# Kernel optimization log

Measured on AMD Instinct MI355X. Metric: run time of the kernel, lower is better.

The kernel has to match this reference:

```python
import jax, jax.numpy as jnp
import numpy as np

L, D, V, BS, H, HD, DL = 12, 768, 50257, 1024, 12, 64, 256
B, T = 2, 1024
EPS = 1e-5


def _ln(x, w, b):
    m = jnp.mean(x, axis=-1, keepdims=True)
    v = jnp.mean((x - m) ** 2, axis=-1, keepdims=True)
    return (x - m) * jax.lax.rsqrt(v + EPS) * w + b


def _rope_tables(t_len):
    inv_freq = 1.0 / (10000.0 ** (jnp.arange(0, HD, 2, dtype=jnp.float32) / HD))
    t = jnp.arange(t_len, dtype=jnp.float32)
    freqs = jnp.outer(t, inv_freq)  # [T, HD/2]
    return jnp.cos(freqs), jnp.sin(freqs)


def _apply_rope(x, cos, sin):
    # x: [B, H, T, HD]; cos/sin: [T, HD/2]
    c = jnp.concatenate([cos, cos], axis=-1)[None, None]
    s = jnp.concatenate([sin, sin], axis=-1)[None, None]
    x1, x2 = jnp.split(x, 2, axis=-1)
    rot = jnp.concatenate([-x2, x1], axis=-1)
    return x * c + rot * s


def setup_inputs() -> dict:
    key = jax.random.key(0)
    ks = jax.random.split(key, 16)
    std = 0.02
    n = lambda k, shape: jax.random.normal(k, shape, dtype=jnp.float32) * std
    return {
        'idx': jax.random.randint(ks[0], (B, T), 0, V),
        'wte': n(ks[1], (V, D)),
        'wpe': n(ks[2], (BS, D)),
        'ln1_w': jnp.ones((L, D)), 'ln1_b': jnp.zeros((L, D)),
        'wq_w': n(ks[3], (L, D, H * HD)), 'wq_b': jnp.zeros((L, H * HD)),
        'kva_w': n(ks[4], (L, D, DL)), 'kva_b': jnp.zeros((L, DL)),
        'kvb_w': n(ks[5], (L, DL, 2 * H * HD)), 'kvb_b': jnp.zeros((L, 2 * H * HD)),
        'out_w': n(ks[6], (L, H * HD, D)), 'out_b': jnp.zeros((L, D)),
        'ln2_w': jnp.ones((L, D)), 'ln2_b': jnp.zeros((L, D)),
        'fc_w': n(ks[7], (L, D, 4 * D)), 'fc_b': jnp.zeros((L, 4 * D)),
        'proj_w': n(ks[8], (L, 4 * D, D)), 'proj_b': jnp.zeros((L, D)),
        'lnf_w': jnp.ones((D,)), 'lnf_b': jnp.zeros((D,)),
    }


def _forward(idx, wte, wpe, ln1_w, ln1_b, wq_w, wq_b, kva_w, kva_b, kvb_w, kvb_b,
             out_w, out_b, ln2_w, ln2_b, fc_w, fc_b, proj_w, proj_b, lnf_w, lnf_b):
    b, t = idx.shape
    x = wte[idx] + wpe[:t][None]  # [B,T,D]
    cos, sin = _rope_tables(t)
    scale = 1.0 / np.sqrt(HD)
    causal = jnp.tril(jnp.ones((t, t), dtype=bool))
    for l in range(L):
        h = _ln(x, ln1_w[l], ln1_b[l])
        q = (h @ wq_w[l] + wq_b[l]).reshape(b, t, H, HD).transpose(0, 2, 1, 3)
        kv_latent = h @ kva_w[l] + kva_b[l]  # [B,T,DL] (the cacheable latent)
        kv = (kv_latent @ kvb_w[l] + kvb_b[l]).reshape(b, t, 2, H, HD)
        kv = kv.transpose(2, 0, 3, 1, 4)  # [2,B,H,T,HD]
        k, v = kv[0], kv[1]
        q = _apply_rope(q, cos, sin)
        k = _apply_rope(k, cos, sin)
        scores = jnp.einsum('bhtd,bhsd->bhts', q, k) * scale
        scores = jnp.where(causal[None, None], scores, -jnp.inf)
        probs = jax.nn.softmax(scores, axis=-1)
        attn = jnp.einsum('bhts,bhsd->bhtd', probs, v)
        attn = attn.transpose(0, 2, 1, 3).reshape(b, t, H * HD)
        x = x + attn @ out_w[l] + out_b[l]
        h2 = _ln(x, ln2_w[l], ln2_b[l])
        mlp = jax.nn.gelu(h2 @ fc_w[l] + fc_b[l], approximate=False) @ proj_w[l] + proj_b[l]
        x = x + mlp
    x = _ln(x, lnf_w, lnf_b)
    logits = x @ wte.T  # tied lm_head
    return logits


def reference(idx, wte, wpe, ln1_w, ln1_b, wq_w, wq_b, kva_w, kva_b, kvb_w, kvb_b,
              out_w, out_b, ln2_w, ln2_b, fc_w, fc_b, proj_w, proj_b, lnf_w, lnf_b):
    return _forward(idx, wte, wpe, ln1_w, ln1_b, wq_w, wq_b, kva_w, kva_b, kvb_w,
                    kvb_b, out_w, out_b, ln2_w, ln2_b, fc_w, fc_b, proj_w, proj_b,
                    lnf_w, lnf_b)
```

## Files before the change

kernel.cpp:

```cpp
#include <hip/hip_runtime.h>
#include <cstdint>
#include <cstddef>


typedef unsigned short ushortT;
typedef __bf16 bf16x8 __attribute__((ext_vector_type(8)));
typedef float f32x4 __attribute__((ext_vector_type(4)));

#define NHEAD 12
#define T_SEQ 1024

__device__ __forceinline__ float bf2f(unsigned short u) {
    union { unsigned int i; float f; } v; v.i = ((unsigned int)u) << 16; return v.f;
}
__device__ __forceinline__ unsigned short f2bf(float f) {
    union { float f; unsigned int i; } v; v.f = f;
    unsigned int r = v.i + 0x7fffu + ((v.i >> 16) & 1u);
    return (unsigned short)(r >> 16);
}
__device__ __forceinline__ unsigned int pack2(float a, float b) {
    return (unsigned int)f2bf(a) | ((unsigned int)f2bf(b) << 16);
}
__device__ __forceinline__ void gload_lds16(const void* g, void* l) {
    __builtin_amdgcn_global_load_lds((__attribute__((address_space(1))) void*)g,
                                     (__attribute__((address_space(3))) void*)l, 16, 0, 0);
}
template <int N>
__device__ __forceinline__ void wait_vmcnt() {
    if constexpr (N == 8)      asm volatile("s_waitcnt vmcnt(8)" ::: "memory");
    else if constexpr (N == 6) asm volatile("s_waitcnt vmcnt(6)" ::: "memory");
    else if constexpr (N == 4) asm volatile("s_waitcnt vmcnt(4)" ::: "memory");
    else                       asm volatile("s_waitcnt vmcnt(0)" ::: "memory");
}

__global__ __launch_bounds__(256) void transpose_cvt_kernel(
    const float* __restrict__ in, ushortT* __restrict__ outp,
    int K, int N, int outRowOff, size_t outLS) {
    __shared__ float tile[32][33];
    const int tid = threadIdx.x;
    const int n0 = blockIdx.x * 32, k0 = blockIdx.y * 32;
    const float* src = in + (size_t)blockIdx.z * K * N;
    {
        const int r = tid >> 3, cg = tid & 7;
        float4 v = *(const float4*)(src + (size_t)(k0 + r) * N + n0 + cg * 4);
        tile[r][cg * 4 + 0] = v.x; tile[r][cg * 4 + 1] = v.y;
        tile[r][cg * 4 + 2] = v.z; tile[r][cg * 4 + 3] = v.w;
    }
    __syncthreads();
    {
        const int nr = tid >> 3, kg = tid & 7;
        ushort4 o;
        o.x = f2bf(tile[kg * 4 + 0][nr]);
        o.y = f2bf(tile[kg * 4 + 1][nr]);
        o.z = f2bf(tile[kg * 4 + 2][nr]);
        o.w = f2bf(tile[kg * 4 + 3][nr]);
        ushortT* dst = outp + (size_t)blockIdx.z * outLS;
        *(ushort4*)(dst + (size_t)(outRowOff + n0 + nr) * K + k0 + kg * 4) = o;
    }
}

__global__ void cvt_wte_kernel(const float* __restrict__ in, ushortT* __restrict__ outp) {
    size_t i4 = (size_t)blockIdx.x * 256 + threadIdx.x;
    ushort4 o;
    if (i4 < 9649344) {
        float4 v = ((const float4*)in)[i4];
        o.x = f2bf(v.x); o.y = f2bf(v.y); o.z = f2bf(v.z); o.w = f2bf(v.w);
    } else { o.x = 0; o.y = 0; o.z = 0; o.w = 0; }
    ((ushort4*)outp)[i4] = o;
}

__global__ void embed_kernel(const int* __restrict__ idx, const float* __restrict__ wte,
                             const float* __restrict__ wpe, float* __restrict__ x) {
    int i = blockIdx.x * 256 + threadIdx.x;
    int row = i / 768, d = i - row * 768;
    int t = row & 1023;
    x[i] = wte[(size_t)idx[row] * 768 + d] + wpe[(size_t)t * 768 + d];
}

__global__ void rope_tables_kernel(float* __restrict__ cosT, float* __restrict__ sinT) {
    int i = blockIdx.x * 256 + threadIdx.x;
    int t = i >> 5, f = i & 31;
    float invf = exp2f(-(float)f * (13.287712379549449f / 32.0f));
    float ang = (float)t * invf;
    cosT[i] = cosf(ang);
    sinT[i] = sinf(ang);
}

__global__ __launch_bounds__(256) void ln_kernel(const float* __restrict__ x,
                                                 const float* __restrict__ wg,
                                                 const float* __restrict__ bg,
                                                 ushortT* __restrict__ outp) {
    const int row = blockIdx.x, tid = threadIdx.x;
    const float* xr = x + (size_t)row * 768;
    float v0 = xr[tid], v1 = xr[tid + 256], v2 = xr[tid + 512];
    float s = v0 + v1 + v2;
    float ss = v0 * v0 + v1 * v1 + v2 * v2;
#pragma unroll
    for (int off = 32; off >= 1; off >>= 1) {
        s += __shfl_xor(s, off);
        ss += __shfl_xor(ss, off);
    }
    __shared__ float sb[4], ssb[4];
    if ((tid & 63) == 0) { sb[tid >> 6] = s; ssb[tid >> 6] = ss; }
    __syncthreads();
    float S = sb[0] + sb[1] + sb[2] + sb[3];
    float SS = ssb[0] + ssb[1] + ssb[2] + ssb[3];
    const float mean = S * (1.0f / 768.0f);
    float var = SS * (1.0f / 768.0f) - mean * mean;
    const float rs = rsqrtf(var + 1e-5f);
    ushortT* orow = outp + (size_t)row * 768;
    orow[tid]       = f2bf((v0 - mean) * rs * wg[tid]       + bg[tid]);
    orow[tid + 256] = f2bf((v1 - mean) * rs * wg[tid + 256] + bg[tid + 256]);
    orow[tid + 512] = f2bf((v2 - mean) * rs * wg[tid + 512] + bg[tid + 512]);
}

template <int BM, int NF, int NTHR, bool ROPE>
__global__ __launch_bounds__(NTHR) void gemmT(
    const ushortT* __restrict__ A, int lda,
    const ushortT* __restrict__ Bt, int ldb,
    int K, int CS, int Nstore,
    const float* __restrict__ bias0, const float* __restrict__ bias1,
    ushortT* __restrict__ outB0, int ld0,
    ushortT* __restrict__ outB1, int ld1, int mode1,
    const float* __restrict__ resid, float* __restrict__ outF, int ldF,
    int act, const float* __restrict__ cosT, const float* __restrict__ sinT) {
    constexpr int WC = (NTHR == 512) ? 4 : 2;
    constexpr int WMR = BM / 2;
    constexpr int MF = WMR / 16;
    constexpr int NFh = NF / WC;
    constexpr int WNh = NFh * 16;
    constexpr int ABYTES = BM * 128;
    constexpr int BBYTES = NF * 2048;
    constexpr int BUFB = ABYTES + BBYTES;
    constexpr int A_LOADS = (BM * 8) / NTHR;
    constexpr int B_LOADS = (NF * 128) / NTHR;
    constexpr int S = A_LOADS + B_LOADS;
    __shared__ __align__(16) char lds[2 * BUFB];
    const int tid = threadIdx.x;
    const int w = tid >> 6, lane = tid & 63;
    const int wm = w / WC, wn = w % WC;
    const int gx = gridDim.x;
    const int nwg = gx * gridDim.y;
    const int flat = blockIdx.x + gx * blockIdx.y;
    const int xcd = flat & 7, loc = flat >> 3;
    const int qq = nwg >> 3, rr_ = nwg & 7;
    const int swz = (xcd < rr_ ? xcd * (qq + 1) : rr_ * (qq + 1) + (xcd - rr_) * qq) + loc;
    const int m0 = (swz % gx) * BM, n0 = (swz / gx) * NF * 16;
    const int fr = lane & 15, kg = lane >> 4;
    const size_t ldaB = (size_t)lda * 2, ldbB = (size_t)ldb * 2;
    const char* Ab = (const char*)A;
    const char* Bb = (const char*)Bt;
    f32x4 acc[MF][NFh] = {};

    auto stage = [&](int buf, int t) {
        const size_t ktB = (size_t)t << 7;
        char* As_ = lds + buf * BUFB;
        char* Bs_ = As_ + ABYTES;
#pragma unroll
        for (int jj = 0; jj < A_LOADS; ++jj) {
            const int i = tid + jj * NTHR;
            const int r = i >> 3, c = i & 7, cc = c ^ (r & 7);
            gload_lds16(Ab + (size_t)(m0 + r) * ldaB + ktB + cc * 16, As_ + i * 16);
        }
#pragma unroll
        for (int jj = 0; jj < B_LOADS; ++jj) {
            const int i = tid + jj * NTHR;
            const int r = i >> 3, c = i & 7, cc = c ^ (r & 7);
            gload_lds16(Bb + (size_t)(n0 + r) * ldbB + ktB + cc * 16, Bs_ + i * 16);
        }
    };

    const int nk = K >> 6;
    stage(0, 0);
    if (nk > 1) { stage(1, 1); wait_vmcnt<S>(); }
    else        { wait_vmcnt<0>(); }
    __builtin_amdgcn_s_barrier();

    for (int t = 0; t < nk; ++t) {
        const int cur = t & 1;
        const char* As_ = lds + cur * BUFB;
        const char* Bs_ = As_ + ABYTES;
        bf16x8 af[MF][2], bfr[NFh][2];
#pragma unroll
        for (int mf = 0; mf < MF; ++mf) {
            const int row = wm * WMR + mf * 16 + fr;
#pragma unroll
            for (int ks = 0; ks < 2; ++ks)
                af[mf][ks] = *(const bf16x8*)(As_ + row * 128 + (((ks * 4 + kg) ^ (row & 7)) << 4));
        }
#pragma unroll
        for (int nf = 0; nf < NFh; ++nf) {
            const int row = wn * WNh + nf * 16 + fr;
#pragma unroll
            for (int ks = 0; ks < 2; ++ks)
                bfr[nf][ks] = *(const bf16x8*)(Bs_ + row * 128 + (((ks * 4 + kg) ^ (row & 7)) << 4));
        }
        if (t + 2 < nk) {
            asm volatile("s_waitcnt lgkmcnt(0)" ::: "memory");
            __builtin_amdgcn_s_barrier();
            stage(cur, t + 2);
        }
#pragma unroll
        for (int ks = 0; ks < 2; ++ks)
#pragma unroll
            for (int nf = 0; nf < NFh; ++nf)
#pragma unroll
                for (int mf = 0; mf < MF; ++mf)
                    acc[mf][nf] = __builtin_amdgcn_mfma_f32_16x16x32_bf16(
                        af[mf][ks], bfr[nf][ks], acc[mf][nf], 0, 0, 0);
        if (t + 1 < nk) {
            if (t + 2 < nk) wait_vmcnt<S>();
            else            wait_vmcnt<0>();
            __builtin_amdgcn_s_barrier();
        }
    }

    if constexpr (ROPE) {
        float vv[MF][4][4];
#pragma unroll
        for (int mf = 0; mf < MF; ++mf)
#pragma unroll
            for (int nf = 0; nf < 4; ++nf) {
                const int gcol = n0 + wn * 64 + nf * 16 + fr;
                float bv = (gcol < CS) ? (bias0 ? bias0[gcol] : 0.0f)
                                       : (bias1 ? bias1[gcol - CS] : 0.0f);
#pragma unroll
                for (int j = 0; j < 4; ++j) vv[mf][nf][j] = acc[mf][nf][j] + bv;
            }
        if (n0 + wn * 64 < 768) {
#pragma unroll
            for (int mf = 0; mf < MF; ++mf)
#pragma unroll
                for (int j = 0; j < 4; ++j) {
                    const int grow = m0 + wm * WMR + mf * 16 + kg * 4 + j;
                    const int t = grow & 1023;
                    const float c0 = cosT[t * 32 + fr],      s0 = sinT[t * 32 + fr];
                    const float c1 = cosT[t * 32 + 16 + fr], s1 = sinT[t * 32 + 16 + fr];
                    float x1 = vv[mf][0][j], x2 = vv[mf][2][j];
                    vv[mf][0][j] = x1 * c0 - x2 * s0;
                    vv[mf][2][j] = x2 * c0 + x1 * s0;
                    float y1 = vv[mf][1][j], y2 = vv[mf][3][j];
                    vv[mf][1][j] = y1 * c1 - y2 * s1;
                    vv[mf][3][j] = y2 * c1 + y1 * s1;
                }
        }
#pragma unroll
        for (int mf = 0; mf < MF; ++mf)
#pragma unroll
            for (int nf = 0; nf < 4; ++nf) {
                const int gcol = n0 + wn * 64 + nf * 16 + fr;
                if (gcol >= Nstore) continue;
#pragma unroll
                for (int j = 0; j < 4; ++j) {
                    const int grow = m0 + wm * WMR + mf * 16 + kg * 4 + j;
                    const float v = vv[mf][nf][j];
                    if (gcol < CS) {
                        if (outB0) outB0[(size_t)grow * ld0 + gcol] = f2bf(v);
                    } else if (outB1) {
                        if (mode1 == 0) {
                            outB1[(size_t)grow * ld1 + gcol - CS] = f2bf(v);
                        } else {
                            const int bb = grow >> 10, tt = grow & 1023;
                            const int hd = gcol - CS;
                            outB1[((size_t)((bb * 12 + (hd >> 6)) * 64 + (hd & 63)) << 10) + tt] = f2bf(v);
                        }
                    }
                }
            }
    } else {
#pragma unroll
        for (int mf = 0; mf < MF; ++mf) {
#pragma unroll
            for (int nf = 0; nf < NFh; ++nf) {
                const int gcol = n0 + wn * WNh + nf * 16 + fr;
                if (gcol >= Nstore) continue;
                float bv = 0.0f;
                if (gcol < CS) { if (bias0) bv = bias0[gcol]; }
                else           { if (bias1) bv = bias1[gcol - CS]; }
#pragma unroll
                for (int j = 0; j < 4; ++j) {
                    const int grow = m0 + wm * WMR + mf * 16 + kg * 4 + j;
                    float v = acc[mf][nf][j] + bv;
                    if (resid) v += resid[(size_t)grow * ldF + gcol];
                    if (act) v = 0.5f * v * (1.0f + erff(v * 0.70710678118654752f));
                    if (outF) outF[(size_t)grow * ldF + gcol] = v;
                    if (gcol < CS) {
                        if (outB0) outB0[(size_t)grow * ld0 + gcol] = f2bf(v);
                    } else if (outB1) {
                        if (mode1 == 0) {
                            outB1[(size_t)grow * ld1 + gcol - CS] = f2bf(v);
                        } else {
                            const int bb = grow >> 10, tt = grow & 1023;
                            const int hd = gcol - CS;
                            outB1[((size_t)((bb * 12 + (hd >> 6)) * 64 + (hd & 63)) << 10) + tt] = f2bf(v);
                        }
                    }
                }
            }
        }
    }
}

#define LM_PHASE(SLOT, MB, STAGE_STMT, TAILWAIT)                              \
    {                                                                          \
        bf16x8 af[2][2];                                                       \
        _Pragma("unroll") for (int m = 0; m < 2; ++m)                          \
        _Pragma("unroll") for (int ks = 0; ks < 2; ++ks) {                     \
            const int row = (MB + m) * 16 + fr;                                \
            af[m][ks] = *(const bf16x8*)(Aw + (SLOT) * 32768 + row * 128 +     \
                                         (((ks * 4 + kg) ^ (row & 7)) << 4));  \
        }                                                                      \
        STAGE_STMT;                                                            \
        __builtin_amdgcn_s_barrier();                                          \
        asm volatile("s_waitcnt lgkmcnt(0)" ::: "memory");                     \
        __builtin_amdgcn_sched_barrier(0);                                     \
        __builtin_amdgcn_s_setprio(1);                                         \
        _Pragma("unroll") for (int ks = 0; ks < 2; ++ks)                       \
        _Pragma("unroll") for (int nf = 0; nf < 4; ++nf)                       \
        _Pragma("unroll") for (int m = 0; m < 2; ++m)                          \
            acc[MB + m][nf] = __builtin_amdgcn_mfma_f32_16x16x32_bf16(         \
                af[m][ks], bfr[nf][ks], acc[MB + m][nf], 0, 0, 0);             \
        __builtin_amdgcn_s_setprio(0);                                         \
        TAILWAIT;                                                              \
        __builtin_amdgcn_s_barrier();                                          \
    }

__global__ __launch_bounds__(512, 1) void lmhead8(
    const ushortT* __restrict__ A, const ushortT* __restrict__ Bt,
    float* __restrict__ outF) {
    __shared__ __align__(16) char lds[131072];
    const int tid = threadIdx.x;
    const int w = tid >> 6, lane = tid & 63;
    const int wm = w >> 2, wn = w & 3;
    const int fr = lane & 15, kg = lane >> 4;
    const int flat = blockIdx.x + 8 * blockIdx.y;
    const int swz = (flat & 7) * 197 + (flat >> 3);
    const int m0 = (swz & 7) * 256, n0 = (swz >> 3) * 256;

    const char* Ag = (const char*)A;
    const char* Bg = (const char*)Bt;
    const char* Aw = lds + wm * 16384;
    const char* Bw = lds + 65536 + (wn >> 1) * 16384;
    const int brow0 = (wn & 1) * 64;

    auto stA = [&](int tile, int half) {
        char* dst = lds + (tile & 1) * 32768 + half * 16384;
#pragma unroll
        for (int jj = 0; jj < 2; ++jj) {
            const int i = tid + jj * 512;
            const int r = i >> 3, c = i & 7, cc = c ^ (r & 7);
            gload_lds16(Ag + (size_t)(m0 + half * 128 + r) * 1536 + tile * 128 + cc * 16,
                        dst + i * 16);
        }
    };
    auto stB = [&](int tile, int half) {
        char* dst = lds + 65536 + (tile & 1) * 32768 + half * 16384;
#pragma unroll
        for (int jj = 0; jj < 2; ++jj) {
            const int i = tid + jj * 512;
            const int r = i >> 3, c = i & 7, cc = c ^ (r & 7);
            gload_lds16(Bg + (size_t)(n0 + half * 128 + r) * 1536 + tile * 128 + cc * 16,
                        dst + i * 16);
        }
    };

    f32x4 acc[8][4] = {};
    stA(0, 0); stA(0, 1); stB(0, 0); stB(0, 1); stB(1, 0); stB(1, 1);
    wait_vmcnt<4>();
    __builtin_amdgcn_s_barrier();

    for (int i = 0; i < 6; ++i) {
        const int t1 = 2 * i + 1;
        const bool st = (i < 5);
        bf16x8 bfr[4][2];
#pragma unroll
        for (int nf = 0; nf < 4; ++nf)
#pragma unroll
            for (int ks = 0; ks < 2; ++ks) {
                const int row = brow0 + nf * 16 + fr;
                bfr[nf][ks] = *(const bf16x8*)(Bw + 0 * 32768 + row * 128 +
                                               (((ks * 4 + kg) ^ (row & 7)) << 4));
            }
        LM_PHASE(0, 0, stA(t1, 0), )
        LM_PHASE(0, 2, stA(t1, 1), )
        LM_PHASE(0, 4, if (st) stB(t1 + 1, 0), )
        LM_PHASE(0, 6, if (st) stB(t1 + 1, 1),
                 if (st) { wait_vmcnt<4>(); } else { wait_vmcnt<0>(); }
                 __builtin_amdgcn_sched_barrier(0))
#pragma unroll
        for (int nf = 0; nf < 4; ++nf)
#pragma unroll
            for (int ks = 0; ks < 2; ++ks) {
                const int row = brow0 + nf * 16 + fr;
                bfr[nf][ks] = *(const bf16x8*)(Bw + 1 * 32768 + row * 128 +
                                               (((ks * 4 + kg) ^ (row & 7)) << 4));
            }
        LM_PHASE(1, 0, if (st) stA(t1 + 1, 0), )
        LM_PHASE(1, 2, if (st) stA(t1 + 1, 1), )
        LM_PHASE(1, 4, if (st) stB(t1 + 2, 0), )
        LM_PHASE(1, 6, if (st) stB(t1 + 2, 1),
                 if (st) { wait_vmcnt<4>(); } else { wait_vmcnt<0>(); }
                 __builtin_amdgcn_sched_barrier(0))
    }

#pragma unroll
    for (int mf = 0; mf < 8; ++mf)
#pragma unroll
        for (int nf = 0; nf < 4; ++nf) {
            const int col = n0 + wn * 64 + nf * 16 + fr;
            if (col < 50257) {
#pragma unroll
                for (int j = 0; j < 4; ++j) {
                    const int row = m0 + wm * 128 + mf * 16 + kg * 4 + j;
                    outF[(size_t)row * 50257 + col] = acc[mf][nf][j];
                }
            }
        }
}

__global__ __launch_bounds__(256) void attn_mfma(const ushortT* __restrict__ q,
                                                 const ushortT* __restrict__ kbuf,
                                                 const ushortT* __restrict__ vT,
                                                 ushortT* __restrict__ attnb) {
    __shared__ __align__(16) char lds[41472];
    const int tid = threadIdx.x, w = tid >> 6, lane = tid & 63;
    const int fr = lane & 15, kg = lane >> 4;
    const int b = blockIdx.y / NHEAD, h = blockIdx.y % NHEAD;
    const int qb = blockIdx.x * 64;
    const int q0 = qb + w * 16;
    const int nst = (qb >> 6) + 1, diag = qb >> 6;

    const ushortT* qrow = q + ((size_t)(b * 1024 + q0 + fr) * 768 + h * 64);
    const bf16x8 qf0 = *(const bf16x8*)(qrow + kg * 8);
    const bf16x8 qf1 = *(const bf16x8*)(qrow + 32 + kg * 8);

    const char* kgb = (const char*)kbuf + ((size_t)(b * 1024) * 768 + h * 64) * 2;
    const char* vgb = (const char*)vT + ((size_t)(b * 12 + h) * 65536) * 2;
    char* Pw = lds + 32768 + w * 2176 + fr * 136;

    auto stage = [&](int buf, int st) {
#pragma unroll
        for (int jj = 0; jj < 2; ++jj) {
            const int i = tid + jj * 256;
            const int r = i >> 3, c = i & 7, cc = c ^ (r & 7);
            gload_lds16(kgb + (size_t)(st * 64 + r) * 1536 + cc * 16, lds + buf * 8192 + i * 16);
            gload_lds16(vgb + (size_t)r * 2048 + st * 128 + cc * 16, lds + 16384 + buf * 8192 + i * 16);
        }
    };

    float m_r = -1e30f, l_r = 0.0f;
    f32x4 o[4] = {};

    stage(0, 0);
    if (nst > 1) stage(1, 1);
    for (int st = 0; st < nst; ++st) {
        const int cur = st & 1;
        if (st + 1 < nst) wait_vmcnt<4>();
        else              wait_vmcnt<0>();
        __builtin_amdgcn_s_barrier();
        const char* Kd = lds + cur * 8192;
        const char* Vd = lds + 16384 + cur * 8192;

        f32x4 sfr[4];
        __builtin_amdgcn_s_setprio(1);
#pragma unroll
        for (int n = 0; n < 4; ++n) {
            const int row = n * 16 + fr;
            bf16x8 k0 = *(const bf16x8*)(Kd + row * 128 + ((kg ^ (row & 7)) << 4));
            bf16x8 k1 = *(const bf16x8*)(Kd + row * 128 + (((4 + kg) ^ (row & 7)) << 4));
            f32x4 sa = {0.0f, 0.0f, 0.0f, 0.0f};
            sa = __builtin_amdgcn_mfma_f32_16x16x32_bf16(k0, qf0, sa, 0, 0, 0);
            sa = __builtin_amdgcn_mfma_f32_16x16x32_bf16(k1, qf1, sa, 0, 0, 0);
            sfr[n] = sa;
        }
        __builtin_amdgcn_s_setprio(0);
        const int qoff = w * 16 + fr;
#pragma unroll
        for (int n = 0; n < 4; ++n)
#pragma unroll
            for (int j = 0; j < 4; ++j) {
                float v = sfr[n][j] * 0.125f;
                if (st == diag && (n * 16 + kg * 4 + j) > qoff) v = -1e30f;
                sfr[n][j] = v;
            }
        float tm = -1e30f;
#pragma unroll
        for (int n = 0; n < 4; ++n)
#pragma unroll
            for (int j = 0; j < 4; ++j) tm = fmaxf(tm, sfr[n][j]);
        tm = fmaxf(tm, __shfl_xor(tm, 16));
        tm = fmaxf(tm, __shfl_xor(tm, 32));
        const float mnew = fmaxf(m_r, tm);
        const float fac = __expf(m_r - mnew);
        m_r = mnew;
        l_r *= fac;
        const float ff0 = __shfl(fac, kg * 4 + 0);
        const float ff1 = __shfl(fac, kg * 4 + 1);
        const float ff2 = __shfl(fac, kg * 4 + 2);
        const float ff3 = __shfl(fac, kg * 4 + 3);
#pragma unroll
        for (int nf = 0; nf < 4; ++nf) {
            o[nf][0] *= ff0; o[nf][1] *= ff1; o[nf][2] *= ff2; o[nf][3] *= ff3;
        }
#pragma unroll
        for (int n = 0; n < 4; ++n) {
            float e0 = __expf(sfr[n][0] - mnew);
            float e1 = __expf(sfr[n][1] - mnew);
            float e2 = __expf(sfr[n][2] - mnew);
            float e3 = __expf(sfr[n][3] - mnew);
            l_r += (e0 + e1) + (e2 + e3);
            uint2 pv;
            pv.x = pack2(e0, e1);
            pv.y = pack2(e2, e3);
            *(uint2*)(Pw + n * 32 + kg * 8) = pv;
        }
        __builtin_amdgcn_s_setprio(1);
#pragma unroll
        for (int ks = 0; ks < 2; ++ks) {
            uint2 a0 = *(const uint2*)(Pw + ks * 64 + kg * 16);
            uint2 a1 = *(const uint2*)(Pw + ks * 64 + kg * 16 + 8);
            union { uint4 u; bf16x8 v; } pa;
            pa.u = make_uint4(a0.x, a0.y, a1.x, a1.y);
#pragma unroll
            for (int nf = 0; nf < 4; ++nf) {
                const int row = nf * 16 + fr;
                bf16x8 vf = *(const bf16x8*)(Vd + row * 128 + (((ks * 4 + kg) ^ (row & 7)) << 4));
                o[nf] = __builtin_amdgcn_mfma_f32_16x16x32_bf16(pa.v, vf, o[nf], 0, 0, 0);
            }
        }
        __builtin_amdgcn_s_setprio(0);
        __builtin_amdgcn_s_barrier();
        if (st + 2 < nst) stage(cur, st + 2);
    }

    l_r += __shfl_xor(l_r, 16);
    l_r += __shfl_xor(l_r, 32);
    const float inv = 1.0f / l_r;
    const float iv0 = __shfl(inv, kg * 4 + 0);
    const float iv1 = __shfl(inv, kg * 4 + 1);
    const float iv2 = __shfl(inv, kg * 4 + 2);
    const float iv3 = __shfl(inv, kg * 4 + 3);
#pragma unroll
    for (int nf = 0; nf < 4; ++nf) {
        const size_t base = (size_t)(b * 1024 + q0) * 768 + h * 64 + nf * 16 + fr;
        attnb[base + (size_t)(kg * 4 + 0) * 768] = f2bf(o[nf][0] * iv0);
        attnb[base + (size_t)(kg * 4 + 1) * 768] = f2bf(o[nf][1] * iv1);
        attnb[base + (size_t)(kg * 4 + 2) * 768] = f2bf(o[nf][2] * iv2);
        attnb[base + (size_t)(kg * 4 + 3) * 768] = f2bf(o[nf][3] * iv3);
    }
}

extern "C" void kernel_launch(void* const* d_in, const int* in_sizes, int n_in,
                              void* d_out, int out_size, void* d_ws, size_t ws_size,
                              hipStream_t stream) {
    (void)in_sizes; (void)n_in; (void)out_size; (void)ws_size;
    const int*   idxp   = (const int*)d_in[0];
    const float* wte    = (const float*)d_in[1];
    const float* wpe    = (const float*)d_in[2];
    const float* ln1_w  = (const float*)d_in[3];
    const float* ln1_b  = (const float*)d_in[4];
    const float* wq_w   = (const float*)d_in[5];
    const float* wq_b   = (const float*)d_in[6];
    const float* kva_w  = (const float*)d_in[7];
    const float* kva_b  = (const float*)d_in[8];
    const float* kvb_w  = (const float*)d_in[9];
    const float* kvb_b  = (const float*)d_in[10];
    const float* out_w  = (const float*)d_in[11];
    const float* out_b  = (const float*)d_in[12];
    const float* ln2_w  = (const float*)d_in[13];
    const float* ln2_b  = (const float*)d_in[14];
    const float* fc_w   = (const float*)d_in[15];
    const float* fc_b   = (const float*)d_in[16];
    const float* proj_w = (const float*)d_in[17];
    const float* proj_b = (const float*)d_in[18];
    const float* lnf_w  = (const float*)d_in[19];
    const float* lnf_b  = (const float*)d_in[20];

    char* ws = (char*)d_ws;
    size_t off = 0;
    auto alloc = [&](size_t bytes) -> char* {
        char* p = ws + off;
        off += (bytes + 255) & ~(size_t)255;
        return p;
    };
    ushortT* wqkvaT = (ushortT*)alloc((size_t)12 * 1024 * 768 * 2);
    ushortT* kvbT   = (ushortT*)alloc((size_t)12 * 1536 * 256 * 2);
    ushortT* outT   = (ushortT*)alloc((size_t)12 * 768 * 768 * 2);
    ushortT* fcT    = (ushortT*)alloc((size_t)12 * 3072 * 768 * 2);
    ushortT* projT  = (ushortT*)alloc((size_t)12 * 768 * 3072 * 2);
    ushortT* wteB   = (ushortT*)alloc((size_t)50432 * 768 * 2);
    float* cosT = (float*)alloc((size_t)1024 * 32 * 4);
    float* sinT = (float*)alloc((size_t)1024 * 32 * 4);
    float*   x     = (float*)alloc((size_t)2048 * 768 * 4);
    ushortT* h     = (ushortT*)alloc((size_t)2048 * 768 * 2);
    ushortT* qbuf  = (ushortT*)alloc((size_t)2048 * 768 * 2);
    ushortT* lat   = (ushortT*)alloc((size_t)2048 * 256 * 2);
    ushortT* kvbuf = (ushortT*)alloc((size_t)2048 * 768 * 2);
    ushortT* vTb   = (ushortT*)alloc((size_t)24 * 64 * 1024 * 2);
    ushortT* attnb = (ushortT*)alloc((size_t)2048 * 768 * 2);
    ushortT* fca   = (ushortT*)alloc((size_t)2048 * 3072 * 2);

    transpose_cvt_kernel<<<dim3(24, 24, 12), 256, 0, stream>>>(wq_w,  wqkvaT, 768, 768,  0,   (size_t)1024 * 768);
    transpose_cvt_kernel<<<dim3(8,  24, 12), 256, 0, stream>>>(kva_w, wqkvaT, 768, 256,  768, (size_t)1024 * 768);
    transpose_cvt_kernel<<<dim3(48, 8,  12), 256, 0, stream>>>(kvb_w, kvbT,   256, 1536, 0,   (size_t)1536 * 256);
    transpose_cvt_kernel<<<dim3(24, 24, 12), 256, 0, stream>>>(out_w, outT,   768, 768,  0,   (size_t)768 * 768);
    transpose_cvt_kernel<<<dim3(96, 24, 12), 256, 0, stream>>>(fc_w,  fcT,    768, 3072, 0,   (size_t)3072 * 768);
    transpose_cvt_kernel<<<dim3(24, 96, 12), 256, 0, stream>>>(proj_w, projT, 3072, 768, 0,   (size_t)768 * 3072);
    cvt_wte_kernel<<<37824, 256, 0, stream>>>(wte, wteB);
    rope_tables_kernel<<<128, 256, 0, stream>>>(cosT, sinT);
    embed_kernel<<<6144, 256, 0, stream>>>(idxp, wte, wpe, x);

    for (int l = 0; l < 12; ++l) {
        ln_kernel<<<2048, 256, 0, stream>>>(x, ln1_w + l * 768, ln1_b + l * 768, h);
        gemmT<64, 8, 256, true><<<dim3(32, 8), 256, 0, stream>>>(
            h, 768, wqkvaT + (size_t)l * 1024 * 768, 768,
            768, 768, 1024, wq_b + l * 768, kva_b + l * 256,
            qbuf, 768, lat, 256, 0, nullptr, nullptr, 0, 0, cosT, sinT);
        gemmT<64, 8, 256, true><<<dim3(32, 12), 256, 0, stream>>>(
            lat, 256, kvbT + (size_t)l * 1536 * 256, 256,
            256, 768, 1536, kvb_b + l * 1536, kvb_b + l * 1536 + 768,
            kvbuf, 768, vTb, 0, 1, nullptr, nullptr, 0, 0, cosT, sinT);
        attn_mfma<<<dim3(16, 24), 256, 0, stream>>>(qbuf, kvbuf, vTb, attnb);
        gemmT<64, 8, 256, false><<<dim3(32, 6), 256, 0, stream>>>(
            attnb, 768, outT + (size_t)l * 768 * 768, 768,
            768, 768, 768, out_b + l * 768, nullptr,
            nullptr, 0, nullptr, 0, 0, x, x, 768, 0, nullptr, nullptr);
        ln_kernel<<<2048, 256, 0, stream>>>(x, ln2_w + l * 768, ln2_b + l * 768, h);
        gemmT<128, 12, 512, false><<<dim3(16, 16), 512, 0, stream>>>(
            h, 768, fcT + (size_t)l * 3072 * 768, 768,
            768, 3072, 3072, fc_b + l * 3072, nullptr,
            fca, 3072, nullptr, 0, 0, nullptr, nullptr, 0, 1, nullptr, nullptr);
        gemmT<64, 8, 256, false><<<dim3(32, 6), 256, 0, stream>>>(
            fca, 3072, projT + (size_t)l * 768 * 3072, 3072,
            3072, 768, 768, proj_b + l * 768, nullptr,
            nullptr, 0, nullptr, 0, 0, x, x, 768, 0, nullptr, nullptr);
    }
    ln_kernel<<<2048, 256, 0, stream>>>(x, lnf_w, lnf_b, h);
    lmhead8<<<dim3(8, 197), 512, 0, stream>>>(h, wteB, (float*)d_out);
}
```

Measured before the change: 2.133 ms.

## Split-K the out and proj GEMMs and fuse the partial reduce with LayerNorm

The out-projection and MLP down-projection GEMMs now split K across 2 and 4 z-slices and write fp32 partials into a scratch buffer. A new reduce_ln kernel sums the partials, bias and residual into x and applies the following LayerNorm in the same pass, which replaces the separate ln_kernel launches. The goal is to fill more CUs than the 192-block grids did and to remove one pass over x for each LayerNorm. It also remaps the attention blocks so each XCD gets contiguous heads and the heaviest causal query blocks start first. The cost is extra global traffic for the partial buffers.

```diff
diff --git a/kernel.cpp b/kernel.cpp
--- a/kernel.cpp
+++ b/kernel.cpp
@@ -29,6 +29,7 @@
 __device__ __forceinline__ void wait_vmcnt() {
     if constexpr (N == 8)      asm volatile("s_waitcnt vmcnt(8)" ::: "memory");
     else if constexpr (N == 6) asm volatile("s_waitcnt vmcnt(6)" ::: "memory");
+    else if constexpr (N == 5) asm volatile("s_waitcnt vmcnt(5)" ::: "memory");
     else if constexpr (N == 4) asm volatile("s_waitcnt vmcnt(4)" ::: "memory");
     else                       asm volatile("s_waitcnt vmcnt(0)" ::: "memory");
 }
@@ -114,7 +115,54 @@
     orow[tid + 512] = f2bf((v2 - mean) * rs * wg[tid + 512] + bg[tid + 512]);
 }
 
-template <int BM, int NF, int NTHR, bool ROPE>
+template <int NP>
+__global__ __launch_bounds__(256) void reduce_ln_kernel(
+    float* __restrict__ x, const float* __restrict__ part,
+    const float* __restrict__ bias,
+    const float* __restrict__ wg, const float* __restrict__ bg,
+    ushortT* __restrict__ outp) {
+    const int row = blockIdx.x, tid = threadIdx.x;
+    const size_t base = (size_t)row * 768;
+    float4 v = {0.f, 0.f, 0.f, 0.f};
+    if (tid < 192) {
+        v = *(const float4*)(x + base + tid * 4);
+        const float4 b4 = *(const float4*)(bias + tid * 4);
+        v.x += b4.x; v.y += b4.y; v.z += b4.z; v.w += b4.w;
+#pragma unroll
+        for (int p = 0; p < NP; ++p) {
+            const float4 pv = *(const float4*)(part + (size_t)p * 1572864 + base + tid * 4);
+            v.x += pv.x; v.y += pv.y; v.z += pv.z; v.w += pv.w;
+        }
+        *(float4*)(x + base + tid * 4) = v;
+    }
+    float s = v.x + v.y + v.z + v.w;
+    float ss = v.x * v.x + v.y * v.y + v.z * v.z + v.w * v.w;
+#pragma unroll
+    for (int off = 32; off >= 1; off >>= 1) {
+        s += __shfl_xor(s, off);
+        ss += __shfl_xor(ss, off);
+    }
+    __shared__ float sb[4], ssb[4];
+    if ((tid & 63) == 0) { sb[tid >> 6] = s; ssb[tid >> 6] = ss; }
+    __syncthreads();
+    const float S = sb[0] + sb[1] + sb[2] + sb[3];
+    const float SS = ssb[0] + ssb[1] + ssb[2] + ssb[3];
+    const float mean = S * (1.0f / 768.0f);
+    const float var = SS * (1.0f / 768.0f) - mean * mean;
+    const float rs = rsqrtf(var + 1e-5f);
+    if (tid < 192) {
+        const float4 w4 = *(const float4*)(wg + tid * 4);
+        const float4 g4 = *(const float4*)(bg + tid * 4);
+        ushort4 o;
+        o.x = f2bf((v.x - mean) * rs * w4.x + g4.x);
+        o.y = f2bf((v.y - mean) * rs * w4.y + g4.y);
+        o.z = f2bf((v.z - mean) * rs * w4.z + g4.z);
+        o.w = f2bf((v.w - mean) * rs * w4.w + g4.w);
+        *(ushort4*)(outp + base + tid * 4) = o;
+    }
+}
+
+template <int BM, int NF, int NTHR, bool ROPE, bool PARTIAL = false>
 __global__ __launch_bounds__(NTHR) void gemmT(
     const ushortT* __restrict__ A, int lda,
     const ushortT* __restrict__ Bt, int ldb,
@@ -148,8 +196,12 @@
     const int m0 = (swz % gx) * BM, n0 = (swz / gx) * NF * 16;
     const int fr = lane & 15, kg = lane >> 4;
     const size_t ldaB = (size_t)lda * 2, ldbB = (size_t)ldb * 2;
-    const char* Ab = (const char*)A;
-    const char* Bb = (const char*)Bt;
+    int koff = 0;
+    if constexpr (PARTIAL) koff = blockIdx.z * K;
+    const char* Ab = (const char*)A + (size_t)koff * 2;
+    const char* Bb = (const char*)Bt + (size_t)koff * 2;
+    float* outFz = outF;
+    if constexpr (PARTIAL) outFz = outF + (size_t)blockIdx.z * 2048 * (size_t)ldF;
     f32x4 acc[MF][NFh] = {};
 
     auto stage = [&](int buf, int t) {
@@ -283,7 +335,7 @@
                     float v = acc[mf][nf][j] + bv;
                     if (resid) v += resid[(size_t)grow * ldF + gcol];
                     if (act) v = 0.5f * v * (1.0f + erff(v * 0.70710678118654752f));
-                    if (outF) outF[(size_t)grow * ldF + gcol] = v;
+                    if (outFz) outFz[(size_t)grow * ldF + gcol] = v;
                     if (gcol < CS) {
                         if (outB0) outB0[(size_t)grow * ld0 + gcol] = f2bf(v);
                     } else if (outB1) {
@@ -425,8 +477,11 @@
     __shared__ __align__(16) char lds[41472];
     const int tid = threadIdx.x, w = tid >> 6, lane = tid & 63;
     const int fr = lane & 15, kg = lane >> 4;
-    const int b = blockIdx.y / NHEAD, h = blockIdx.y % NHEAD;
-    const int qb = blockIdx.x * 64;
+    const int flat = blockIdx.x + 16 * blockIdx.y;
+    const int nf2 = (flat & 7) * 48 + (flat >> 3);
+    const int bh = nf2 >> 4;
+    const int b = bh / NHEAD, h = bh % NHEAD;
+    const int qb = (15 - (nf2 & 15)) * 64;
     const int q0 = qb + w * 16;
     const int nst = (qb >> 6) + 1, diag = qb >> 6;
 
@@ -599,6 +654,7 @@
     ushortT* vTb   = (ushortT*)alloc((size_t)24 * 64 * 1024 * 2);
     ushortT* attnb = (ushortT*)alloc((size_t)2048 * 768 * 2);
     ushortT* fca   = (ushortT*)alloc((size_t)2048 * 3072 * 2);
+    float*   partB = (float*)alloc((size_t)4 * 2048 * 768 * 4);
 
     transpose_cvt_kernel<<<dim3(24, 24, 12), 256, 0, stream>>>(wq_w,  wqkvaT, 768, 768,  0,   (size_t)1024 * 768);
     transpose_cvt_kernel<<<dim3(8,  24, 12), 256, 0, stream>>>(kva_w, wqkvaT, 768, 256,  768, (size_t)1024 * 768);
@@ -609,9 +665,9 @@
     cvt_wte_kernel<<<37824, 256, 0, stream>>>(wte, wteB);
     rope_tables_kernel<<<128, 256, 0, stream>>>(cosT, sinT);
     embed_kernel<<<6144, 256, 0, stream>>>(idxp, wte, wpe, x);
+    ln_kernel<<<2048, 256, 0, stream>>>(x, ln1_w, ln1_b, h);
 
     for (int l = 0; l < 12; ++l) {
-        ln_kernel<<<2048, 256, 0, stream>>>(x, ln1_w + l * 768, ln1_b + l * 768, h);
         gemmT<64, 8, 256, true><<<dim3(32, 8), 256, 0, stream>>>(
             h, 768, wqkvaT + (size_t)l * 1024 * 768, 768,
             768, 768, 1024, wq_b + l * 768, kva_b + l * 256,
@@ -621,20 +677,24 @@
             256, 768, 1536, kvb_b + l * 1536, kvb_b + l * 1536 + 768,
             kvbuf, 768, vTb, 0, 1, nullptr, nullptr, 0, 0, cosT, sinT);
         attn_mfma<<<dim3(16, 24), 256, 0, stream>>>(qbuf, kvbuf, vTb, attnb);
-        gemmT<64, 8, 256, false><<<dim3(32, 6), 256, 0, stream>>>(
+        gemmT<64, 8, 256, false, true><<<dim3(32, 6, 2), 256, 0, stream>>>(
             attnb, 768, outT + (size_t)l * 768 * 768, 768,
-            768, 768, 768, out_b + l * 768, nullptr,
-            nullptr, 0, nullptr, 0, 0, x, x, 768, 0, nullptr, nullptr);
-        ln_kernel<<<2048, 256, 0, stream>>>(x, ln2_w + l * 768, ln2_b + l * 768, h);
+            384, 768, 768, nullptr, nullptr,
+            nullptr, 0, nullptr, 0, 0, nullptr, partB, 768, 0, nullptr, nullptr);
+        reduce_ln_kernel<2><<<2048, 256, 0, stream>>>(
+            x, partB, out_b + l * 768, ln2_w + l * 768, ln2_b + l * 768, h);
         gemmT<128, 12, 512, false><<<dim3(16, 16), 512, 0, stream>>>(
             h, 768, fcT + (size_t)l * 3072 * 768, 768,
             768, 3072, 3072, fc_b + l * 3072, nullptr,
             fca, 3072, nullptr, 0, 0, nullptr, nullptr, 0, 1, nullptr, nullptr);
-        gemmT<64, 8, 256, false><<<dim3(32, 6), 256, 0, stream>>>(
+        gemmT<64, 8, 256, false, true><<<dim3(32, 6, 4), 256, 0, stream>>>(
             fca, 3072, projT + (size_t)l * 768 * 3072, 3072,
-            3072, 768, 768, proj_b + l * 768, nullptr,
-            nullptr, 0, nullptr, 0, 0, x, x, 768, 0, nullptr, nullptr);
-    }
-    ln_kernel<<<2048, 256, 0, stream>>>(x, lnf_w, lnf_b, h);
+            768, 768, 768, nullptr, nullptr,
+            nullptr, 0, nullptr, 0, 0, nullptr, partB, 768, 0, nullptr, nullptr);
+        const float* nw = (l < 11) ? ln1_w + (l + 1) * 768 : lnf_w;
+        const float* nb = (l < 11) ? ln1_b + (l + 1) * 768 : lnf_b;
+        reduce_ln_kernel<4><<<2048, 256, 0, stream>>>(
+            x, partB, proj_b + l * 768, nw, nb, h);
+    }
     lmhead8<<<dim3(8, 197), 512, 0, stream>>>(h, wteB, (float*)d_out);
 }
```

Result: faster. 1.898 ms (-11.0%).
